# Kernel tuning notes

Hardware: AMD Instinct MI355X
Metric: run time of the kernel (lower is better)

## Reference

```python
import jax, jax.numpy as jnp
import numpy as np
import math

B, S, HID = 2, 2048, 2048
NH, NKV = 32, 8
HD = HID // NH  # 64
N_REP = NH // NKV  # 4


def setup_inputs() -> dict:
    key = jax.random.key(0)
    ks = jax.random.split(key, 7)
    sc = 0.02
    return {
        "hidden_states": jax.random.normal(ks[0], (B, S, HID), jnp.float32),
        "cos": jax.random.normal(ks[1], (S, HD), jnp.float32),
        "sin": jax.random.normal(ks[2], (S, HD), jnp.float32),
        "wq": jax.random.normal(ks[3], (NH * HD, HID), jnp.float32) * sc,
        "wk": jax.random.normal(ks[4], (NKV * HD, HID), jnp.float32) * sc,
        "wv": jax.random.normal(ks[5], (NKV * HD, HID), jnp.float32) * sc,
        "wo": jax.random.normal(ks[6], (HID, NH * HD), jnp.float32) * sc,
    }


def _rotate_half(x):
    x1, x2 = jnp.split(x, 2, axis=-1)
    return jnp.concatenate([-x2, x1], axis=-1)


def _apply_rotary(q, k, cos, sin):
    # q: [B,S,NH,HD], k: [B,S,NKV,HD]; cos/sin: [S,HD] broadcast over batch, heads
    c = cos[None, :, None, :]
    s = sin[None, :, None, :]
    return q * c + _rotate_half(q) * s, k * c + _rotate_half(k) * s


def reference(hidden_states, cos, sin, wq, wk, wv, wo):
    x = hidden_states  # [B,S,HID]
    q = jnp.einsum('bsh,dh->bsd', x, wq).reshape(B, S, NH, HD)
    k = jnp.einsum('bsh,dh->bsd', x, wk).reshape(B, S, NKV, HD)
    v = jnp.einsum('bsh,dh->bsd', x, wv).reshape(B, S, NKV, HD)
    q, k = _apply_rotary(q, k, cos, sin)
    # repeat_kv: expand kv heads by N_REP -> [B,S,NH,HD]
    k = jnp.repeat(k, N_REP, axis=2)
    v = jnp.repeat(v, N_REP, axis=2)
    # [B,NH,S,HD]
    q = q.transpose(0, 2, 1, 3)
    k = k.transpose(0, 2, 1, 3)
    v = v.transpose(0, 2, 1, 3)
    scores = jnp.einsum('bhqd,bhkd->bhqk', q, k) / math.sqrt(HD)
    probs = jax.nn.softmax(scores.astype(jnp.float32), axis=-1).astype(q.dtype)
    out = jnp.einsum('bhqk,bhkd->bhqd', probs, v)
    out = out.transpose(0, 2, 1, 3).reshape(B, S, NH * HD)
    return jnp.einsum('bsd,hd->bsh', out, wo)
```

## Files before the change

kernel.cpp:

```cpp
#include <hip/hip_runtime.h>
#include <math.h>

#define B 2
#define S 2048
#define HID 2048
#define NH 32
#define NKV 8
#define HD 64
#define NREP 4

typedef __bf16 bf16_t;
typedef bf16_t bf16x8 __attribute__((ext_vector_type(8)));
typedef bf16_t bf16x4 __attribute__((ext_vector_type(4)));
typedef bf16_t bf16x2 __attribute__((ext_vector_type(2)));
typedef float floatx4 __attribute__((ext_vector_type(4)));

__device__ __forceinline__ void gld_lds16(const void* g, void* l) {
    __builtin_amdgcn_global_load_lds(
        (const __attribute__((address_space(1))) void*)g,
        (__attribute__((address_space(3))) void*)l, 16, 0, 0);
}

__device__ __forceinline__ int pack2(float a, float b) {
    bf16x2 v; v[0] = (bf16_t)a; v[1] = (bf16_t)b;
    return __builtin_bit_cast(int, v);
}

__device__ __forceinline__ bf16x8 cat8i(int2 lo, int2 hi) {
    int4 w; w.x = lo.x; w.y = lo.y; w.z = hi.x; w.w = hi.y;
    return __builtin_bit_cast(bf16x8, w);
}

__global__ __launch_bounds__(256) void cast_all(const float* __restrict__ x,
                                                const float* __restrict__ wq,
                                                const float* __restrict__ wk,
                                                const float* __restrict__ wv,
                                                const float* __restrict__ wo,
                                                bf16_t* __restrict__ xb,
                                                bf16_t* __restrict__ wqkvb,
                                                bf16_t* __restrict__ wob) {
    int gid = blockIdx.x * 256 + threadIdx.x;
    const float* src; bf16_t* dst; int idx;
    if (gid < 1048576)      { src = x;  dst = xb;               idx = gid; }
    else if (gid < 1572864) { src = wq; dst = wqkvb;            idx = gid - 1048576; }
    else if (gid < 1703936) { src = wk; dst = wqkvb + 4194304;  idx = gid - 1572864; }
    else if (gid < 1835008) { src = wv; dst = wqkvb + 5242880;  idx = gid - 1703936; }
    else                    { src = wo; dst = wob;              idx = gid - 1835008; }
    size_t i = (size_t)idx * 8;
    float4 f0 = *(const float4*)(src + i);
    float4 f1 = *(const float4*)(src + i + 4);
    bf16x8 v;
    v[0] = (bf16_t)f0.x; v[1] = (bf16_t)f0.y; v[2] = (bf16_t)f0.z; v[3] = (bf16_t)f0.w;
    v[4] = (bf16_t)f1.x; v[5] = (bf16_t)f1.y; v[6] = (bf16_t)f1.z; v[7] = (bf16_t)f1.w;
    *(bf16x8*)(dst + i) = v;
}

#define TM 128
#define TN 128
#define BK 64

enum { MODE_QKV = 0, MODE_OUT = 2 };

template <int MODE>
__global__ __launch_bounds__(256) void gemm_mfma(const bf16_t* __restrict__ A,
                                                 const bf16_t* __restrict__ W,
                                                 void* __restrict__ outQ,
                                                 bf16_t* __restrict__ outK,
                                                 bf16_t* __restrict__ outV,
                                                 const float* __restrict__ cosp,
                                                 const float* __restrict__ sinp,
                                                 int M, int N, int K) {
    __shared__ __align__(16) bf16_t As[2 * TM * 32];
    __shared__ __align__(16) bf16_t Ws[2 * TN * 32];
    const int t    = threadIdx.x;
    const int wave = t >> 6, lane = t & 63;
    const int quad = lane >> 4, l16 = lane & 15;
    const int gx   = gridDim.x;
    const int nwg  = gx * gridDim.y;
    const int flat = blockIdx.y * gx + blockIdx.x;
    const int rm   = (flat & 7) * (nwg >> 3) + (flat >> 3);
    const int m0 = (rm / gx) * TM, n0 = (rm % gx) * TN;
    const int wm = (wave >> 1) * 64, wn = (wave & 1) * 64;

    floatx4 zero4 = {0.f, 0.f, 0.f, 0.f};
    floatx4 acc[4][4];
    #pragma unroll
    for (int i = 0; i < 4; ++i)
        #pragma unroll
        for (int j = 0; j < 4; ++j) acc[i][j] = zero4;

    const int r4 = t >> 2;
    const int c8 = (t & 3) * 8;
    const bf16_t* Arow = A + (size_t)(m0 + r4) * K + c8;
    const bf16_t* Wrow = W + (size_t)(n0 + r4) * K + c8;

    for (int k0 = 0; k0 < K; k0 += BK) {
        #pragma unroll
        for (int ks = 0; ks < 2; ++ks) {
            gld_lds16(Arow + k0 + ks * 32,          As + ks * 4096 + t * 8);
            gld_lds16(Arow + 64 * K + k0 + ks * 32, As + ks * 4096 + 2048 + t * 8);
            gld_lds16(Wrow + k0 + ks * 32,          Ws + ks * 4096 + t * 8);
            gld_lds16(Wrow + 64 * K + k0 + ks * 32, Ws + ks * 4096 + 2048 + t * 8);
        }
        __syncthreads();
        #pragma unroll
        for (int ks = 0; ks < 2; ++ks) {
            bf16x8 af[4], bfr[4];
            #pragma unroll
            for (int i = 0; i < 4; ++i)
                af[i] = *(bf16x8*)&As[ks * 4096 + (wm + i * 16 + l16) * 32 + quad * 8];
            #pragma unroll
            for (int j = 0; j < 4; ++j)
                bfr[j] = *(bf16x8*)&Ws[ks * 4096 + (wn + j * 16 + l16) * 32 + quad * 8];
            #pragma unroll
            for (int i = 0; i < 4; ++i)
                #pragma unroll
                for (int j = 0; j < 4; ++j)
                    acc[i][j] = __builtin_amdgcn_mfma_f32_16x16x32_bf16(af[i], bfr[j], acc[i][j], 0, 0, 0);
        }
        __syncthreads();
    }

    if constexpr (MODE == MODE_OUT) {
        float* C = (float*)outQ;
        #pragma unroll
        for (int i = 0; i < 4; ++i)
            #pragma unroll
            for (int r = 0; r < 4; ++r) {
                int row = m0 + wm + i * 16 + quad * 4 + r;
                #pragma unroll
                for (int j = 0; j < 4; ++j)
                    C[(size_t)row * N + n0 + wn + j * 16 + l16] = acc[i][j][r];
            }
    } else {
        const int hh = (n0 + wn) / 64;
        #pragma unroll
        for (int i = 0; i < 4; ++i)
            #pragma unroll
            for (int r = 0; r < 4; ++r) {
                int m = m0 + wm + i * 16 + quad * 4 + r;
                int b = m / S, s = m % S;
                if (hh < NH + NKV) {
                    bf16_t* base;
                    float sc;
                    if (hh < NH) {
                        base = (bf16_t*)outQ + ((size_t)(b * NH + hh) * S + s) * HD;
                        sc = 0.18033688011f;
                    } else {
                        base = outK + ((size_t)(b * NKV + (hh - NH)) * S + s) * HD;
                        sc = 1.0f;
                    }
                    #pragma unroll
                    for (int j = 0; j < 2; ++j) {
                        int d = j * 16 + l16;
                        float x1 = acc[i][j][r], x2 = acc[i][j + 2][r];
                        float c1 = cosp[s * HD + d],      s1 = sinp[s * HD + d];
                        float c2 = cosp[s * HD + d + 32], s2 = sinp[s * HD + d + 32];
                        base[d]      = (bf16_t)((x1 * c1 - x2 * s1) * sc);
                        base[d + 32] = (bf16_t)((x2 * c2 + x1 * s2) * sc);
                    }
                } else {
                    int kvh = hh - NH - NKV;
                    int w  = s & 63, lo = w & 31;
                    int pos = (lo < 16) ? (((lo >> 2) << 3) | (lo & 3))
                                        : ((((lo - 16) >> 2) << 3) | 4 | (lo & 3));
                    int ps = (s & ~63) | ((w & 32) + pos);
                    bf16_t* vb = outV + ((size_t)(b * NKV + kvh) * HD) * S + ps;
                    #pragma unroll
                    for (int j = 0; j < 4; ++j)
                        vb[(size_t)(j * 16 + l16) * S] = (bf16_t)acc[i][j][r];
                }
            }
    }
}

__global__ __launch_bounds__(256, 4) void attn_mfma(const bf16_t* __restrict__ Q,
                                                    const bf16_t* __restrict__ Kb,
                                                    const bf16_t* __restrict__ Vt,
                                                    bf16_t* __restrict__ Ob) {
    __shared__ __align__(16) bf16_t Ks[2 * 64 * 32];
    __shared__ __align__(16) bf16_t Vs[2 * 64 * 32];
    const int t    = threadIdx.x;
    const int wave = t >> 6, lane = t & 63;
    const int quad = lane >> 4, l16 = lane & 15;

    const int flat  = blockIdx.y * 16 + blockIdx.x;
    const int local = flat >> 3;
    const int combo = (flat & 7) * 2 + (local >> 6);
    const int b = combo >> 3, kvh = combo & 7;
    const int h  = kvh * NREP + ((local >> 4) & 3);
    const int q0 = (local & 15) * 128;
    const int bh = b * NH + h;

    const bf16_t* qbase = Q + ((size_t)bh * S + q0 + wave * 32) * HD;
    const bf16_t* kbase = Kb + ((size_t)(b * NKV + kvh) * S) * HD;
    const bf16_t* vbase = Vt + (size_t)(b * NKV + kvh) * HD * S;

    bf16x8 qf[2][2];
    #pragma unroll
    for (int qj = 0; qj < 2; ++qj)
        #pragma unroll
        for (int ks = 0; ks < 2; ++ks)
            qf[qj][ks] = *(const bf16x8*)(qbase + (size_t)(qj * 16 + l16) * HD + ks * 32 + quad * 8);

    floatx4 zero4 = {0.f, 0.f, 0.f, 0.f};
    floatx4 of[4][2];
    #pragma unroll
    for (int di = 0; di < 4; ++di)
        #pragma unroll
        for (int qj = 0; qj < 2; ++qj) of[di][qj] = zero4;
    float lsum[2] = {0.f, 0.f};

    const int r4 = t >> 2;
    const int c8 = (t & 3) * 8;

    #pragma unroll
    for (int ks = 0; ks < 2; ++ks)
        gld_lds16(kbase + (size_t)r4 * HD + ks * 32 + c8, Ks + ks * 2048 + t * 8);
    __syncthreads();

    for (int kt = 0; kt < S; kt += 64) {
        #pragma unroll
        for (int ks = 0; ks < 2; ++ks)
            gld_lds16(vbase + (size_t)r4 * S + kt + ks * 32 + c8, Vs + ks * 2048 + t * 8);

        int2 pk[4][2];
        #pragma unroll
        for (int ki = 0; ki < 4; ++ki) {
            bf16x8 ka0 = *(bf16x8*)&Ks[0 * 2048 + (ki * 16 + l16) * 32 + quad * 8];
            bf16x8 ka1 = *(bf16x8*)&Ks[1 * 2048 + (ki * 16 + l16) * 32 + quad * 8];
            floatx4 sf[2];
            #pragma unroll
            for (int qj = 0; qj < 2; ++qj) sf[qj] = zero4;
            __builtin_amdgcn_s_setprio(1);
            #pragma unroll
            for (int qj = 0; qj < 2; ++qj)
                sf[qj] = __builtin_amdgcn_mfma_f32_16x16x32_bf16(ka0, qf[qj][0], sf[qj], 0, 0, 0);
            #pragma unroll
            for (int qj = 0; qj < 2; ++qj)
                sf[qj] = __builtin_amdgcn_mfma_f32_16x16x32_bf16(ka1, qf[qj][1], sf[qj], 0, 0, 0);
            __builtin_amdgcn_s_setprio(0);
            #pragma unroll
            for (int qj = 0; qj < 2; ++qj) {
                float p0 = __builtin_amdgcn_exp2f(sf[qj][0]);
                float p1 = __builtin_amdgcn_exp2f(sf[qj][1]);
                float p2 = __builtin_amdgcn_exp2f(sf[qj][2]);
                float p3 = __builtin_amdgcn_exp2f(sf[qj][3]);
                lsum[qj] += (p0 + p1) + (p2 + p3);
                pk[ki][qj].x = pack2(p0, p1);
                pk[ki][qj].y = pack2(p2, p3);
            }
        }
        __syncthreads();

        if (kt + 64 < S) {
            #pragma unroll
            for (int ks = 0; ks < 2; ++ks)
                gld_lds16(kbase + (size_t)(kt + 64 + r4) * HD + ks * 32 + c8, Ks + ks * 2048 + t * 8);
        }
        #pragma unroll
        for (int ks = 0; ks < 2; ++ks) {
            __builtin_amdgcn_s_setprio(1);
            #pragma unroll
            for (int di = 0; di < 4; ++di) {
                bf16x8 va = *(bf16x8*)&Vs[ks * 2048 + (di * 16 + l16) * 32 + quad * 8];
                #pragma unroll
                for (int qj = 0; qj < 2; ++qj) {
                    bf16x8 pb = cat8i(pk[2 * ks][qj], pk[2 * ks + 1][qj]);
                    of[di][qj] = __builtin_amdgcn_mfma_f32_16x16x32_bf16(va, pb, of[di][qj], 0, 0, 0);
                }
            }
            __builtin_amdgcn_s_setprio(0);
        }
        __syncthreads();
    }

    #pragma unroll
    for (int qj = 0; qj < 2; ++qj) {
        float ls = lsum[qj];
        ls += __shfl_xor(ls, 16);
        ls += __shfl_xor(ls, 32);
        float inv = 1.f / ls;
        int q = q0 + wave * 32 + qj * 16 + l16;
        bf16_t* ob = Ob + ((size_t)(b * S + q)) * HID + h * HD;
        #pragma unroll
        for (int di = 0; di < 4; ++di) {
            int2 pkv;
            pkv.x = pack2(of[di][qj][0] * inv, of[di][qj][1] * inv);
            pkv.y = pack2(of[di][qj][2] * inv, of[di][qj][3] * inv);
            *(int2*)(ob + di * 16 + quad * 4) = pkv;
        }
    }
}

extern "C" void kernel_launch(void* const* d_in, const int* in_sizes, int n_in,
                              void* d_out, int out_size, void* d_ws, size_t ws_size,
                              hipStream_t stream) {
    const float* x    = (const float*)d_in[0];
    const float* cosp = (const float*)d_in[1];
    const float* sinp = (const float*)d_in[2];
    const float* wq   = (const float*)d_in[3];
    const float* wk   = (const float*)d_in[4];
    const float* wv   = (const float*)d_in[5];
    const float* wo   = (const float*)d_in[6];
    float* out = (float*)d_out;

    char* ws = (char*)d_ws;
    bf16_t* xb    = (bf16_t*)(ws);
    bf16_t* kb    = (bf16_t*)(ws + 16777216);
    bf16_t* vtb   = (bf16_t*)(ws + 20971520);
    bf16_t* wqkvb = (bf16_t*)(ws + 25165824);
    bf16_t* wob   = (bf16_t*)(ws + 37748736);
    bf16_t* attb  = (bf16_t*)(ws);
    bf16_t* qb    = (bf16_t*)d_out;

    const int M = B * S;

    cast_all<<<9216, 256, 0, stream>>>(x, wq, wk, wv, wo, xb, wqkvb, wob);

    gemm_mfma<MODE_QKV><<<dim3(3072 / TN, M / TM), 256, 0, stream>>>(
        xb, wqkvb, (void*)qb, kb, vtb, cosp, sinp, M, 3072, HID);

    attn_mfma<<<dim3(S / 128, B * NH), 256, 0, stream>>>(qb, kb, vtb, attb);

    gemm_mfma<MODE_OUT><<<dim3(2048 / TN, M / TM), 256, 0, stream>>>(
        attb, wob, (void*)out, nullptr, nullptr, nullptr, nullptr, M, 2048, HID);
}
```

Before: 306.2 us.

## Add dedicated 8-wave 256x128 output-projection GEMM with ping-pong scheduling

```diff
diff --git a/kernel.cpp b/kernel.cpp
--- a/kernel.cpp
+++ b/kernel.cpp
@@ -174,6 +174,114 @@
     }
 }
 
+__global__ __launch_bounds__(512, 2) void gemm8_out(const bf16_t* __restrict__ A,
+                                                    const bf16_t* __restrict__ W,
+                                                    float* __restrict__ C) {
+    __shared__ __align__(16) bf16_t As[2][2][256][32];
+    __shared__ __align__(16) bf16_t Bs[2][2][128][32];
+    const int t    = threadIdx.x;
+    const int wave = t >> 6, lane = t & 63;
+    const int quad = lane >> 4, l16 = lane & 15;
+    const int wm = (wave >> 2) * 128;
+    const int wn = (wave & 3) * 32;
+    const int m0 = blockIdx.y * 256, n0 = blockIdx.x * 128;
+    const int KK = HID;
+    const int NN = 2048;
+
+    floatx4 zero4 = {0.f, 0.f, 0.f, 0.f};
+    floatx4 acc[8][2];
+    #pragma unroll
+    for (int i = 0; i < 8; ++i) { acc[i][0] = zero4; acc[i][1] = zero4; }
+
+    const int sr = t >> 2, sc = (t & 3) * 8;
+    const bf16_t* Abase = A + (size_t)(m0 + sr) * KK + sc;
+    const bf16_t* Wbase = W + (size_t)(n0 + sr) * KK + sc;
+
+#define STAGE_A(buf, p, tt) do {                                            \
+        const bf16_t* g_ = Abase + (tt) * 64 + (p) * 32;                    \
+        gld_lds16(g_,            &As[buf][p][0][0] + t * 8);                \
+        gld_lds16(g_ + 128 * KK, &As[buf][p][128][0] + t * 8);              \
+    } while (0)
+#define STAGE_B(buf, p, tt)                                                 \
+        gld_lds16(Wbase + (tt) * 64 + (p) * 32, &Bs[buf][p][0][0] + t * 8)
+#define LDA(buf, p, rf) (*(const bf16x8*)&As[buf][p][wm + (rf) * 16 + l16][quad * 8])
+#define LDB(buf, p, cf) (*(const bf16x8*)&Bs[buf][p][wn + (cf) * 16 + l16][quad * 8])
+#define MFMA8(rbase)                                                        \
+    __builtin_amdgcn_s_setprio(1);                                          \
+    _Pragma("unroll")                                                       \
+    for (int rf = 0; rf < 4; ++rf) {                                        \
+        acc[(rbase) + rf][0] = __builtin_amdgcn_mfma_f32_16x16x32_bf16(     \
+            af[rf], bfr[0], acc[(rbase) + rf][0], 0, 0, 0);                 \
+        acc[(rbase) + rf][1] = __builtin_amdgcn_mfma_f32_16x16x32_bf16(     \
+            af[rf], bfr[1], acc[(rbase) + rf][1], 0, 0, 0);                 \
+    }                                                                       \
+    __builtin_amdgcn_s_setprio(0);
+
+    STAGE_A(0, 0, 0); STAGE_B(0, 0, 0);
+    STAGE_A(0, 1, 0); STAGE_B(0, 1, 0);
+    asm volatile("s_waitcnt vmcnt(3)" ::: "memory");
+    __builtin_amdgcn_s_barrier();
+
+    const int NT = KK / 64;
+    for (int tt = 0; tt < NT; ++tt) {
+        const int buf = tt & 1, nb = buf ^ 1;
+        const bool more = (tt + 1 < NT);
+        bf16x8 af[4], bfr[2];
+
+        bfr[0] = LDB(buf, 0, 0); bfr[1] = LDB(buf, 0, 1);
+        #pragma unroll
+        for (int rf = 0; rf < 4; ++rf) af[rf] = LDA(buf, 0, rf);
+        if (more) STAGE_A(nb, 0, tt + 1);
+        __builtin_amdgcn_s_barrier();
+        MFMA8(0);
+        __builtin_amdgcn_s_barrier();
+
+        #pragma unroll
+        for (int rf = 0; rf < 4; ++rf) af[rf] = LDA(buf, 0, rf + 4);
+        if (more) {
+            STAGE_B(nb, 0, tt + 1);
+            asm volatile("s_waitcnt vmcnt(3)" ::: "memory");
+        } else {
+            asm volatile("s_waitcnt vmcnt(0)" ::: "memory");
+        }
+        __builtin_amdgcn_s_barrier();
+        MFMA8(4);
+        __builtin_amdgcn_s_barrier();
+
+        bfr[0] = LDB(buf, 1, 0); bfr[1] = LDB(buf, 1, 1);
+        #pragma unroll
+        for (int rf = 0; rf < 4; ++rf) af[rf] = LDA(buf, 1, rf);
+        if (more) STAGE_A(nb, 1, tt + 1);
+        __builtin_amdgcn_s_barrier();
+        MFMA8(0);
+        __builtin_amdgcn_s_barrier();
+
+        #pragma unroll
+        for (int rf = 0; rf < 4; ++rf) af[rf] = LDA(buf, 1, rf + 4);
+        if (more) {
+            STAGE_B(nb, 1, tt + 1);
+            asm volatile("s_waitcnt vmcnt(3)" ::: "memory");
+        }
+        __builtin_amdgcn_s_barrier();
+        MFMA8(4);
+        __builtin_amdgcn_s_barrier();
+    }
+#undef STAGE_A
+#undef STAGE_B
+#undef LDA
+#undef LDB
+#undef MFMA8
+
+    #pragma unroll
+    for (int rf = 0; rf < 8; ++rf)
+        #pragma unroll
+        for (int r = 0; r < 4; ++r) {
+            int row = m0 + wm + rf * 16 + quad * 4 + r;
+            C[(size_t)row * NN + n0 + wn + 0 * 16 + l16] = acc[rf][0][r];
+            C[(size_t)row * NN + n0 + wn + 1 * 16 + l16] = acc[rf][1][r];
+        }
+}
+
 __global__ __launch_bounds__(256, 4) void attn_mfma(const bf16_t* __restrict__ Q,
                                                     const bf16_t* __restrict__ Kb,
                                                     const bf16_t* __restrict__ Vt,
@@ -323,6 +431,5 @@
 
     attn_mfma<<<dim3(S / 128, B * NH), 256, 0, stream>>>(qb, kb, vtb, attb);
 
-    gemm_mfma<MODE_OUT><<<dim3(2048 / TN, M / TM), 256, 0, stream>>>(
-        attb, wob, (void*)out, nullptr, nullptr, nullptr, nullptr, M, 2048, HID);
-}
+    gemm8_out<<<dim3(2048 / 128, M / 256), 512, 0, stream>>>(attb, wob, out);
+}
```

Result: no change. 310.1 us (+1.3%).
